# Kernel optimization log

Hardware: AMD Instinct MI355X
Metric: run time of the kernel (lower is better)

## Reference

```python
import jax, jax.numpy as jnp
import numpy as np

T, B, I, H, C, O = 4096, 8, 256, 512, 1024, 512
SCHEDULE = 1.0
UPPER_T = 0.3
NIND = int((1.0 - SCHEDULE) * (C - 2) * UPPER_T) + 1  # = 1 (argmax WTA)


def setup_inputs() -> dict:
    key = jax.random.key(0)
    ks = jax.random.split(key, 8)
    def lin(k, fan_out, fan_in):
        s = 1.0 / np.sqrt(fan_in)
        kw, kb = jax.random.split(k)
        return (jax.random.uniform(kw, (fan_out, fan_in), jnp.float32, -s, s),
                jax.random.uniform(kb, (fan_out,), jnp.float32, -s, s))
    i2m_w, i2m_b = lin(ks[0], H, I)
    m2h_w, m2h_b = lin(ks[1], C, H)
    h2o_w, h2o_b = lin(ks[2], O, C)
    return {
        "x": jax.random.normal(ks[3], (T, B, I), jnp.float32),
        "hidden1": jnp.zeros((1,), jnp.float32),  # unused dummy (overwritten in torch forward)
        "i2m_w": i2m_w, "i2m_b": i2m_b,
        "m2h_w": m2h_w, "m2h_b": m2h_b,
        "h2o_w": h2o_w, "h2o_b": h2o_b,
    }


def reference(x, hidden1, i2m_w, i2m_b, m2h_w, m2h_b, h2o_w, h2o_b):
    # linear -> relu
    h = jax.nn.relu(jnp.einsum('tbi,hi->tbh', x, i2m_w) + i2m_b)
    # linear -> relu -> concept pre-activations [T,B,C]
    c = jax.nn.relu(jnp.einsum('tbh,ch->tbc', h, m2h_w) + m2h_b)
    # winner-take-all: top-Nind scatter mask (replaces CPU argsort round-trip)
    _, idx = jax.lax.top_k(c, NIND)  # [T,B,NIND]
    t_ix = jnp.arange(c.shape[0])[:, None, None]
    b_ix = jnp.arange(c.shape[1])[None, :, None]
    mask = jnp.zeros_like(c).at[t_ix, b_ix, idx].set(1.0)
    m = c * mask
    # L2 normalize over concept axis
    m = m / jnp.linalg.norm(m, axis=-1, keepdims=True)
    out = jnp.einsum('tbc,oc->tbo', m, h2o_w) + h2o_b
    return jax.nn.log_softmax(out, axis=-1)
```

## Files before the change

kernel.cpp:

```cpp
#include <hip/hip_runtime.h>
#include <stdint.h>

#define M_ROWS 32768
#define I_DIM 256
#define H_DIM 512
#define C_DIM 1024
#define O_DIM 512

typedef __attribute__((ext_vector_type(8))) short bf16x8;
typedef __attribute__((ext_vector_type(4))) float f32x4;

__device__ __forceinline__ ushort bf16_rne(float f) {
    unsigned u = __float_as_uint(f);
    unsigned r = u + 0x7FFFu + ((u >> 16) & 1u);
    return (ushort)(r >> 16);
}
__device__ __forceinline__ float bf16_f32(ushort h) {
    return __uint_as_float(((unsigned)h) << 16);
}
__device__ __forceinline__ void split2(float f, ushort& hi, ushort& mid) {
    hi = bf16_rne(f);
    mid = bf16_rne(f - bf16_f32(hi));
}

__device__ __forceinline__ void async_ld16(const void* g, void* l) {
    __builtin_amdgcn_global_load_lds(
        (const __attribute__((address_space(1))) void*)g,
        (__attribute__((address_space(3))) void*)l, 16, 0, 0);
}

__device__ __forceinline__ unsigned long long packvi(float v, int col) {
    unsigned u = __float_as_uint(v);
    u = (u & 0x80000000u) ? ~u : (u | 0x80000000u);
    return ((unsigned long long)u << 32) | (unsigned)(~col);
}

__device__ __forceinline__ int slot_of(int kc, int row) {
    return (kc + ((row >> 1) & 3)) & 3;
}

__global__ __launch_bounds__(256)
void prep(const float* __restrict__ W1, ushort* __restrict__ w1h, ushort* __restrict__ w1m,
          const float* __restrict__ W2, ushort* __restrict__ w2h, ushort* __restrict__ w2m,
          const float* __restrict__ Wo, const float* __restrict__ bo,
          float* __restrict__ LS, unsigned long long* __restrict__ part) {
    __shared__ float sred[4];
    const int b = blockIdx.x;
    const int t = threadIdx.x;
    if (b < 320) {
        const int isW1 = (b < 64);
        const float* W = isW1 ? W1 : W2;
        ushort* hh = isW1 ? w1h : w2h;
        ushort* mm = isW1 ? w1m : w2m;
        const int K = isW1 ? I_DIM : H_DIM;
        const int cpr = K >> 3;
        int gid = (isW1 ? b : b - 64) * 256 + t;
        int row = gid / cpr;
        int rem = gid - row * cpr;
        int g = rem >> 2, kc = rem & 3;
        float4 v0 = *(const float4*)(W + (size_t)gid * 8);
        float4 v1 = *(const float4*)(W + (size_t)gid * 8 + 4);
        __align__(16) ushort h[8], m[8];
        float f[8];
        *(float4*)&f[0] = v0; *(float4*)&f[4] = v1;
        #pragma unroll
        for (int j = 0; j < 8; ++j) split2(f[j], h[j], m[j]);
        size_t dst = (size_t)row * K + g * 32 + slot_of(kc, row) * 8;
        *(uint4*)(hh + dst) = *(uint4*)h;
        *(uint4*)(mm + dst) = *(uint4*)m;
    } else if (b < 1344) {
        const int j = b - 320;
        float l0 = Wo[(size_t)t * C_DIM + j] + bo[t];
        float l1 = Wo[(size_t)(t + 256) * C_DIM + j] + bo[t + 256];

        float mx = fmaxf(l0, l1);
        #pragma unroll
        for (int off = 1; off < 64; off <<= 1)
            mx = fmaxf(mx, __shfl_xor(mx, off, 64));
        if ((t & 63) == 0) sred[t >> 6] = mx;
        __syncthreads();
        mx = fmaxf(fmaxf(sred[0], sred[1]), fmaxf(sred[2], sred[3]));
        __syncthreads();

        float s = expf(l0 - mx) + expf(l1 - mx);
        #pragma unroll
        for (int off = 1; off < 64; off <<= 1)
            s += __shfl_xor(s, off, 64);
        if ((t & 63) == 0) sred[t >> 6] = s;
        __syncthreads();
        s = sred[0] + sred[1] + sred[2] + sred[3];

        float lse = mx + logf(s);
        LS[(size_t)j * O_DIM + t] = l0 - lse;
        LS[(size_t)j * O_DIM + t + 256] = l1 - lse;
    } else {
        part[(b - 1344) * 256 + t] = 0ull;
    }
}

__global__ __launch_bounds__(256, 4)
void gemm1_mfma(const float* __restrict__ X, const ushort* __restrict__ W1h,
                const ushort* __restrict__ W1m, const float* __restrict__ b1,
                ushort* __restrict__ Hh, ushort* __restrict__ Hm) {
    __shared__ __align__(16) ushort LB[16384];
    ushort* As0 = LB;
    ushort* As1 = LB + 4096;
    ushort* Bs0 = LB + 8192;
    ushort* Bs1 = LB + 12288;

    const int tid = threadIdx.x;
    const int lane = tid & 63, wave = tid >> 6;
    const int wm = wave >> 1, wn = wave & 1;
    const int lcol = lane & 15, quad = lane >> 4;
    const int mBase = blockIdx.x * 128;
    const int nBase = blockIdx.y * 128;
    const int s_row = tid >> 1, s_half = tid & 1;
    const int bplane = wave >> 1;
    const ushort* wp = bplane ? W1m : W1h;
    const int brow0 = (wave & 1) * 64;
    const int lrow = lane >> 2, lk = (lane & 3) * 8;

    f32x4 acc[4][4];
    #pragma unroll
    for (int i = 0; i < 4; ++i)
        #pragma unroll
        for (int j = 0; j < 4; ++j)
            acc[i][j] = (f32x4){0.f, 0.f, 0.f, 0.f};

    int aoff[4], boff[4];
    #pragma unroll
    for (int t = 0; t < 4; ++t) {
        int ra = wm * 64 + t * 16 + lcol;
        int rb = wn * 64 + t * 16 + lcol;
        aoff[t] = ra * 32 + slot_of(quad, ra) * 8;
        boff[t] = rb * 32 + slot_of(quad, rb) * 8;
    }
    const int sl0 = slot_of(s_half * 2,     s_row);
    const int sl1 = slot_of(s_half * 2 + 1, s_row);

    for (int ks = 0; ks < I_DIM / 32; ++ks) {
        const int k0 = ks * 32;
        const float* ap = X + (size_t)(mBase + s_row) * I_DIM + k0 + s_half * 16;
        float4 f0 = ((const float4*)ap)[0];
        float4 f1 = ((const float4*)ap)[1];
        float4 f2 = ((const float4*)ap)[2];
        float4 f3 = ((const float4*)ap)[3];

        __syncthreads();

        #pragma unroll
        for (int i = 0; i < 4; ++i) {
            int r = brow0 + i * 16;
            const ushort* g = wp + (size_t)(nBase + r + lrow) * I_DIM + k0 + lk;
            async_ld16(g, (bplane ? Bs1 : Bs0) + r * 32);
        }

        float f[16];
        *(float4*)&f[0] = f0; *(float4*)&f[4] = f1;
        *(float4*)&f[8] = f2; *(float4*)&f[12] = f3;
        bf16x8 h0, h1, m0, m1;
        #pragma unroll
        for (int j = 0; j < 8; ++j) {
            ushort hu, mu;
            split2(f[j], hu, mu);
            h0[j] = (short)hu; m0[j] = (short)mu;
            split2(f[j + 8], hu, mu);
            h1[j] = (short)hu; m1[j] = (short)mu;
        }
        *(bf16x8*)&As0[s_row * 32 + sl0 * 8] = h0;
        *(bf16x8*)&As0[s_row * 32 + sl1 * 8] = h1;
        *(bf16x8*)&As1[s_row * 32 + sl0 * 8] = m0;
        *(bf16x8*)&As1[s_row * 32 + sl1 * 8] = m1;

        __syncthreads();

        bf16x8 af[4][2];
        #pragma unroll
        for (int mt = 0; mt < 4; ++mt) {
            af[mt][0] = *(const bf16x8*)&As0[aoff[mt]];
            af[mt][1] = *(const bf16x8*)&As1[aoff[mt]];
        }
        #pragma unroll
        for (int nt = 0; nt < 4; ++nt) {
            bf16x8 bh = *(const bf16x8*)&Bs0[boff[nt]];
            bf16x8 bm = *(const bf16x8*)&Bs1[boff[nt]];
            #pragma unroll
            for (int mt = 0; mt < 4; ++mt) {
                f32x4 a = acc[mt][nt];
                a = __builtin_amdgcn_mfma_f32_16x16x32_bf16(af[mt][1], bh, a, 0, 0, 0);
                a = __builtin_amdgcn_mfma_f32_16x16x32_bf16(af[mt][0], bm, a, 0, 0, 0);
                a = __builtin_amdgcn_mfma_f32_16x16x32_bf16(af[mt][0], bh, a, 0, 0, 0);
                acc[mt][nt] = a;
            }
        }
    }

    #pragma unroll
    for (int plane = 0; plane < 2; ++plane) {
        __syncthreads();
        #pragma unroll
        for (int nt = 0; nt < 4; ++nt) {
            int colRel = wn * 64 + nt * 16 + lcol;
            int g = colRel >> 5, kc = (colRel >> 3) & 3, pos = colRel & 7;
            float bias = b1[nBase + colRel];
            #pragma unroll
            for (int mt = 0; mt < 4; ++mt) {
                #pragma unroll
                for (int r = 0; r < 4; ++r) {
                    int rowRel = wm * 64 + mt * 16 + quad * 4 + r;
                    float v = fmaxf(acc[mt][nt][r] + bias, 0.f);
                    ushort hu, mu;
                    split2(v, hu, mu);
                    LB[rowRel * 128 + g * 32 + slot_of(kc, rowRel) * 8 + pos]
                        = plane ? mu : hu;
                }
            }
        }
        __syncthreads();
        ushort* dstp = plane ? Hm : Hh;
        #pragma unroll
        for (int l = 0; l < 8; ++l) {
            int c = l * 256 + tid;
            int row = c >> 4, idx = c & 15;
            *(uint4*)(dstp + (size_t)(mBase + row) * H_DIM + nBase + idx * 8)
                = *(const uint4*)&LB[row * 128 + idx * 8];
        }
    }
}

__global__ __launch_bounds__(256, 4)
void gemm2_mfma(const ushort* __restrict__ Hh, const ushort* __restrict__ Hm,
                const ushort* __restrict__ W2h, const ushort* __restrict__ W2m,
                const float* __restrict__ b2,
                unsigned long long* __restrict__ part) {
    __shared__ __align__(16) ushort As[2][128 * 32];
    __shared__ __align__(16) ushort Bs[2][128 * 32];
    const int tid = threadIdx.x;
    const int lane = tid & 63, wave = tid >> 6;
    const int wm = wave >> 1, wn = wave & 1;
    const int lcol = lane & 15, quad = lane >> 4;
    const int mBase = blockIdx.x * 128;
    const int nBase = blockIdx.y * 128;
    const int lrow = lane >> 2, lk = (lane & 3) * 8;

    const ushort* gsrc;
    ushort* lbase;
    switch (wave) {
        case 0: gsrc = Hh  + (size_t)mBase * H_DIM; lbase = As[0]; break;
        case 1: gsrc = Hm  + (size_t)mBase * H_DIM; lbase = As[1]; break;
        case 2: gsrc = W2h + (size_t)nBase * H_DIM; lbase = Bs[0]; break;
        default: gsrc = W2m + (size_t)nBase * H_DIM; lbase = Bs[1]; break;
    }

    f32x4 acc[4][4];
    #pragma unroll
    for (int i = 0; i < 4; ++i)
        #pragma unroll
        for (int j = 0; j < 4; ++j)
            acc[i][j] = (f32x4){0.f, 0.f, 0.f, 0.f};

    int aoff[4], boff[4];
    #pragma unroll
    for (int t = 0; t < 4; ++t) {
        int ra = wm * 64 + t * 16 + lcol;
        int rb = wn * 64 + t * 16 + lcol;
        aoff[t] = ra * 32 + slot_of(quad, ra) * 8;
        boff[t] = rb * 32 + slot_of(quad, rb) * 8;
    }

    for (int ks = 0; ks < H_DIM / 32; ++ks) {
        const int k0 = ks * 32;
        __syncthreads();
        #pragma unroll
        for (int j = 0; j < 8; ++j) {
            const ushort* g = gsrc + (size_t)(j * 16 + lrow) * H_DIM + k0 + lk;
            async_ld16(g, lbase + j * 512);
        }
        __syncthreads();

        bf16x8 af[4][2];
        #pragma unroll
        for (int mt = 0; mt < 4; ++mt) {
            af[mt][0] = *(const bf16x8*)&As[0][aoff[mt]];
            af[mt][1] = *(const bf16x8*)&As[1][aoff[mt]];
        }
        #pragma unroll
        for (int nt = 0; nt < 4; ++nt) {
            bf16x8 bh = *(const bf16x8*)&Bs[0][boff[nt]];
            bf16x8 bm = *(const bf16x8*)&Bs[1][boff[nt]];
            #pragma unroll
            for (int mt = 0; mt < 4; ++mt) {
                f32x4 a = acc[mt][nt];
                a = __builtin_amdgcn_mfma_f32_16x16x32_bf16(af[mt][1], bh, a, 0, 0, 0);
                a = __builtin_amdgcn_mfma_f32_16x16x32_bf16(af[mt][0], bm, a, 0, 0, 0);
                a = __builtin_amdgcn_mfma_f32_16x16x32_bf16(af[mt][0], bh, a, 0, 0, 0);
                acc[mt][nt] = a;
            }
        }
    }

    #pragma unroll
    for (int mt = 0; mt < 4; ++mt) {
        #pragma unroll
        for (int r = 0; r < 4; ++r) {
            unsigned long long best = 0ull;
            #pragma unroll
            for (int nt = 0; nt < 4; ++nt) {
                int col = nBase + wn * 64 + nt * 16 + lcol;
                float v = acc[mt][nt][r] + b2[col];
                unsigned long long p = packvi(v, col);
                if (p > best) best = p;
            }
            #pragma unroll
            for (int off = 1; off < 16; off <<= 1) {
                unsigned long long o = __shfl_xor((long long)best, off, 64);
                if (o > best) best = o;
            }
            if (lcol == 0) {
                int row = mBase + wm * 64 + mt * 16 + quad * 4 + r;
                atomicMax(&part[row], best);
            }
        }
    }
}

__global__ __launch_bounds__(256)
void gather_out(const unsigned long long* __restrict__ part,
                const float* __restrict__ LS, float* __restrict__ out) {
    const int tid = threadIdx.x;
    const int row = blockIdx.x * 2 + (tid >> 7);
    const int q = tid & 127;
    unsigned long long best = part[row];
    unsigned u = (unsigned)(best >> 32);
    float v = (u & 0x80000000u) ? __uint_as_float(u ^ 0x80000000u)
                                : __uint_as_float(~u);
    int col = (int)(~(unsigned)best) & (C_DIM - 1);
    int j = (v > 0.f) ? col : 0;
    float4 val = ((const float4*)LS)[(size_t)j * 128 + q];
    ((float4*)out)[(size_t)row * 128 + q] = val;
}

extern "C" void kernel_launch(void* const* d_in, const int* in_sizes, int n_in,
                              void* d_out, int out_size, void* d_ws, size_t ws_size,
                              hipStream_t stream) {
    const float* x     = (const float*)d_in[0];
    const float* i2m_w = (const float*)d_in[2];
    const float* i2m_b = (const float*)d_in[3];
    const float* m2h_w = (const float*)d_in[4];
    const float* m2h_b = (const float*)d_in[5];
    const float* h2o_w = (const float*)d_in[6];
    const float* h2o_b = (const float*)d_in[7];
    float* out = (float*)d_out;

    char* ws = (char*)d_ws;
    ushort* w1h = (ushort*)(ws);
    ushort* w1m = (ushort*)(ws + 262144);
    ushort* w2h = (ushort*)(ws + 524288);
    ushort* w2m = (ushort*)(ws + 1572864);
    float*  LS  = (float*)(ws + 2621440);
    unsigned long long* part = (unsigned long long*)(ws + 4718592);

    ushort* Hh = (ushort*)d_out;
    ushort* Hm = Hh + (size_t)M_ROWS * H_DIM;

    prep<<<1472, 256, 0, stream>>>(i2m_w, w1h, w1m, m2h_w, w2h, w2m,
                                   h2o_w, h2o_b, LS, part);
    gemm1_mfma<<<dim3(M_ROWS / 128, H_DIM / 128), 256, 0, stream>>>(
        x, w1h, w1m, i2m_b, Hh, Hm);
    gemm2_mfma<<<dim3(M_ROWS / 128, C_DIM / 128), 256, 0, stream>>>(
        Hh, Hm, w2h, w2m, m2h_b, part);
    gather_out<<<M_ROWS / 2, 256, 0, stream>>>(part, LS, out);
}
```

Measured before the change: 253.5 us.

## Double-buffer LDS in both GEMMs, swap grid order, restructure logsoftmax prep

Both MFMA GEMMs now use double-buffered shared memory. The next K-slice is loaded asynchronously, and in gemm1 the next X slice is prefetched into registers, while MFMAs run on the current buffer. This removes one barrier per iteration and overlaps loads with compute. The grid is transposed so that consecutive blocks share the same M rows across N tiles, which should improve L2 reuse of the activation rows. Launch bounds drop to 2 waves/SIMD because LDS use doubles. The output log-softmax table in prep now handles 16 columns per block with coalesced reads, cutting the prep grid from 1472 to 512 blocks.

```diff
diff --git a/kernel.cpp b/kernel.cpp
--- a/kernel.cpp
+++ b/kernel.cpp
@@ -44,7 +44,7 @@
           const float* __restrict__ W2, ushort* __restrict__ w2h, ushort* __restrict__ w2m,
           const float* __restrict__ Wo, const float* __restrict__ bo,
           float* __restrict__ LS, unsigned long long* __restrict__ part) {
-    __shared__ float sred[4];
+    __shared__ float red[16][17];
     const int b = blockIdx.x;
     const int t = threadIdx.x;
     if (b < 320) {
@@ -68,52 +68,58 @@
         size_t dst = (size_t)row * K + g * 32 + slot_of(kc, row) * 8;
         *(uint4*)(hh + dst) = *(uint4*)h;
         *(uint4*)(mm + dst) = *(uint4*)m;
-    } else if (b < 1344) {
-        const int j = b - 320;
-        float l0 = Wo[(size_t)t * C_DIM + j] + bo[t];
-        float l1 = Wo[(size_t)(t + 256) * C_DIM + j] + bo[t + 256];
-
-        float mx = fmaxf(l0, l1);
-        #pragma unroll
-        for (int off = 1; off < 64; off <<= 1)
-            mx = fmaxf(mx, __shfl_xor(mx, off, 64));
-        if ((t & 63) == 0) sred[t >> 6] = mx;
-        __syncthreads();
-        mx = fmaxf(fmaxf(sred[0], sred[1]), fmaxf(sred[2], sred[3]));
-        __syncthreads();
-
-        float s = expf(l0 - mx) + expf(l1 - mx);
-        #pragma unroll
-        for (int off = 1; off < 64; off <<= 1)
-            s += __shfl_xor(s, off, 64);
-        if ((t & 63) == 0) sred[t >> 6] = s;
-        __syncthreads();
-        s = sred[0] + sred[1] + sred[2] + sred[3];
-
-        float lse = mx + logf(s);
-        LS[(size_t)j * O_DIM + t] = l0 - lse;
-        LS[(size_t)j * O_DIM + t + 256] = l1 - lse;
+    } else if (b < 384) {
+        const int j0 = (b - 320) * 16;
+        const int c = t & 15, q = t >> 4;
+        float v[32];
+        float mx = -3.4e38f;
+        #pragma unroll
+        for (int i = 0; i < 32; ++i) {
+            int r = q + 16 * i;
+            v[i] = Wo[(size_t)r * C_DIM + j0 + c] + bo[r];
+            mx = fmaxf(mx, v[i]);
+        }
+        red[q][c] = mx;
+        __syncthreads();
+        #pragma unroll
+        for (int s = 8; s > 0; s >>= 1) {
+            if (q < s) red[q][c] = fmaxf(red[q][c], red[q + s][c]);
+            __syncthreads();
+        }
+        mx = red[0][c];
+        __syncthreads();
+        float sum = 0.f;
+        #pragma unroll
+        for (int i = 0; i < 32; ++i) sum += expf(v[i] - mx);
+        red[q][c] = sum;
+        __syncthreads();
+        #pragma unroll
+        for (int s = 8; s > 0; s >>= 1) {
+            if (q < s) red[q][c] += red[q + s][c];
+            __syncthreads();
+        }
+        float lse = mx + logf(red[0][c]);
+        #pragma unroll
+        for (int i = 0; i < 32; ++i)
+            LS[(size_t)(j0 + c) * O_DIM + q + 16 * i] = v[i] - lse;
     } else {
-        part[(b - 1344) * 256 + t] = 0ull;
-    }
-}
-
-__global__ __launch_bounds__(256, 4)
+        part[(b - 384) * 256 + t] = 0ull;
+    }
+}
+
+__global__ __launch_bounds__(256, 2)
 void gemm1_mfma(const float* __restrict__ X, const ushort* __restrict__ W1h,
                 const ushort* __restrict__ W1m, const float* __restrict__ b1,
                 ushort* __restrict__ Hh, ushort* __restrict__ Hm) {
-    __shared__ __align__(16) ushort LB[16384];
-    ushort* As0 = LB;
-    ushort* As1 = LB + 4096;
-    ushort* Bs0 = LB + 8192;
-    ushort* Bs1 = LB + 12288;
+    __shared__ __align__(16) ushort As[2][2][4096];
+    __shared__ __align__(16) ushort Bs[2][2][4096];
 
     const int tid = threadIdx.x;
     const int lane = tid & 63, wave = tid >> 6;
     const int wm = wave >> 1, wn = wave & 1;
     const int lcol = lane & 15, quad = lane >> 4;
-    const int mBase = blockIdx.x * 128;
-    const int nBase = blockIdx.y * 128;
+    const int nBase = blockIdx.x * 128;
+    const int mBase = blockIdx.y * 128;
     const int s_row = tid >> 1, s_half = tid & 1;
     const int bplane = wave >> 1;
     const ushort* wp = bplane ? W1m : W1h;
@@ -137,27 +143,15 @@
     }
     const int sl0 = slot_of(s_half * 2,     s_row);
     const int sl1 = slot_of(s_half * 2 + 1, s_row);
-
-    for (int ks = 0; ks < I_DIM / 32; ++ks) {
-        const int k0 = ks * 32;
-        const float* ap = X + (size_t)(mBase + s_row) * I_DIM + k0 + s_half * 16;
-        float4 f0 = ((const float4*)ap)[0];
-        float4 f1 = ((const float4*)ap)[1];
-        float4 f2 = ((const float4*)ap)[2];
-        float4 f3 = ((const float4*)ap)[3];
-
-        __syncthreads();
-
-        #pragma unroll
-        for (int i = 0; i < 4; ++i) {
-            int r = brow0 + i * 16;
-            const ushort* g = wp + (size_t)(nBase + r + lrow) * I_DIM + k0 + lk;
-            async_ld16(g, (bplane ? Bs1 : Bs0) + r * 32);
-        }
-
+    const float* xrow = X + (size_t)(mBase + s_row) * I_DIM + s_half * 16;
+
+    float4 xr[2][4];
+    #pragma unroll
+    for (int i = 0; i < 4; ++i) xr[0][i] = ((const float4*)xrow)[i];
+    {
         float f[16];
-        *(float4*)&f[0] = f0; *(float4*)&f[4] = f1;
-        *(float4*)&f[8] = f2; *(float4*)&f[12] = f3;
+        #pragma unroll
+        for (int i = 0; i < 4; ++i) *(float4*)&f[i * 4] = xr[0][i];
         bf16x8 h0, h1, m0, m1;
         #pragma unroll
         for (int j = 0; j < 8; ++j) {
@@ -167,23 +161,64 @@
             split2(f[j + 8], hu, mu);
             h1[j] = (short)hu; m1[j] = (short)mu;
         }
-        *(bf16x8*)&As0[s_row * 32 + sl0 * 8] = h0;
-        *(bf16x8*)&As0[s_row * 32 + sl1 * 8] = h1;
-        *(bf16x8*)&As1[s_row * 32 + sl0 * 8] = m0;
-        *(bf16x8*)&As1[s_row * 32 + sl1 * 8] = m1;
-
-        __syncthreads();
+        *(bf16x8*)&As[0][0][s_row * 32 + sl0 * 8] = h0;
+        *(bf16x8*)&As[0][0][s_row * 32 + sl1 * 8] = h1;
+        *(bf16x8*)&As[0][1][s_row * 32 + sl0 * 8] = m0;
+        *(bf16x8*)&As[0][1][s_row * 32 + sl1 * 8] = m1;
+    }
+    #pragma unroll
+    for (int i = 0; i < 4; ++i) {
+        int r = brow0 + i * 16;
+        async_ld16(wp + (size_t)(nBase + r + lrow) * I_DIM + lk, &Bs[0][bplane][r * 32]);
+    }
+    #pragma unroll
+    for (int i = 0; i < 4; ++i) xr[1][i] = ((const float4*)(xrow + 32))[i];
+
+    #pragma unroll 2
+    for (int ks = 0; ks < 8; ++ks) {
+        const int cur = ks & 1;
+        __syncthreads();
+        if (ks < 7) {
+            const int k0 = (ks + 1) * 32;
+            #pragma unroll
+            for (int i = 0; i < 4; ++i) {
+                int r = brow0 + i * 16;
+                async_ld16(wp + (size_t)(nBase + r + lrow) * I_DIM + k0 + lk,
+                           &Bs[cur ^ 1][bplane][r * 32]);
+            }
+            float f[16];
+            #pragma unroll
+            for (int i = 0; i < 4; ++i) *(float4*)&f[i * 4] = xr[(ks + 1) & 1][i];
+            bf16x8 h0, h1, m0, m1;
+            #pragma unroll
+            for (int j = 0; j < 8; ++j) {
+                ushort hu, mu;
+                split2(f[j], hu, mu);
+                h0[j] = (short)hu; m0[j] = (short)mu;
+                split2(f[j + 8], hu, mu);
+                h1[j] = (short)hu; m1[j] = (short)mu;
+            }
+            *(bf16x8*)&As[cur ^ 1][0][s_row * 32 + sl0 * 8] = h0;
+            *(bf16x8*)&As[cur ^ 1][0][s_row * 32 + sl1 * 8] = h1;
+            *(bf16x8*)&As[cur ^ 1][1][s_row * 32 + sl0 * 8] = m0;
+            *(bf16x8*)&As[cur ^ 1][1][s_row * 32 + sl1 * 8] = m1;
+        }
+        if (ks < 6) {
+            const float* xp = xrow + (ks + 2) * 32;
+            #pragma unroll
+            for (int i = 0; i < 4; ++i) xr[ks & 1][i] = ((const float4*)xp)[i];
+        }
 
         bf16x8 af[4][2];
         #pragma unroll
         for (int mt = 0; mt < 4; ++mt) {
-            af[mt][0] = *(const bf16x8*)&As0[aoff[mt]];
-            af[mt][1] = *(const bf16x8*)&As1[aoff[mt]];
+            af[mt][0] = *(const bf16x8*)&As[cur][0][aoff[mt]];
+            af[mt][1] = *(const bf16x8*)&As[cur][1][aoff[mt]];
         }
         #pragma unroll
         for (int nt = 0; nt < 4; ++nt) {
-            bf16x8 bh = *(const bf16x8*)&Bs0[boff[nt]];
-            bf16x8 bm = *(const bf16x8*)&Bs1[boff[nt]];
+            bf16x8 bh = *(const bf16x8*)&Bs[cur][0][boff[nt]];
+            bf16x8 bm = *(const bf16x8*)&Bs[cur][1][boff[nt]];
             #pragma unroll
             for (int mt = 0; mt < 4; ++mt) {
                 f32x4 a = acc[mt][nt];
@@ -195,6 +230,7 @@
         }
     }
 
+    ushort* LB = &As[0][0][0];
     #pragma unroll
     for (int plane = 0; plane < 2; ++plane) {
         __syncthreads();
@@ -228,28 +264,28 @@
     }
 }
 
-__global__ __launch_bounds__(256, 4)
+__global__ __launch_bounds__(256, 2)
 void gemm2_mfma(const ushort* __restrict__ Hh, const ushort* __restrict__ Hm,
                 const ushort* __restrict__ W2h, const ushort* __restrict__ W2m,
                 const float* __restrict__ b2,
                 unsigned long long* __restrict__ part) {
-    __shared__ __align__(16) ushort As[2][128 * 32];
-    __shared__ __align__(16) ushort Bs[2][128 * 32];
+    __shared__ __align__(16) ushort As[2][2][4096];
+    __shared__ __align__(16) ushort Bs[2][2][4096];
     const int tid = threadIdx.x;
     const int lane = tid & 63, wave = tid >> 6;
     const int wm = wave >> 1, wn = wave & 1;
     const int lcol = lane & 15, quad = lane >> 4;
-    const int mBase = blockIdx.x * 128;
-    const int nBase = blockIdx.y * 128;
+    const int nBase = blockIdx.x * 128;
+    const int mBase = blockIdx.y * 128;
     const int lrow = lane >> 2, lk = (lane & 3) * 8;
 
     const ushort* gsrc;
-    ushort* lbase;
+    ushort *lb0, *lb1;
     switch (wave) {
-        case 0: gsrc = Hh  + (size_t)mBase * H_DIM; lbase = As[0]; break;
-        case 1: gsrc = Hm  + (size_t)mBase * H_DIM; lbase = As[1]; break;
-        case 2: gsrc = W2h + (size_t)nBase * H_DIM; lbase = Bs[0]; break;
-        default: gsrc = W2m + (size_t)nBase * H_DIM; lbase = Bs[1]; break;
+        case 0: gsrc = Hh  + (size_t)mBase * H_DIM; lb0 = As[0][0]; lb1 = As[1][0]; break;
+        case 1: gsrc = Hm  + (size_t)mBase * H_DIM; lb0 = As[0][1]; lb1 = As[1][1]; break;
+        case 2: gsrc = W2h + (size_t)nBase * H_DIM; lb0 = Bs[0][0]; lb1 = Bs[1][0]; break;
+        default: gsrc = W2m + (size_t)nBase * H_DIM; lb0 = Bs[0][1]; lb1 = Bs[1][1]; break;
     }
 
     f32x4 acc[4][4];
@@ -268,26 +304,33 @@
         boff[t] = rb * 32 + slot_of(quad, rb) * 8;
     }
 
-    for (int ks = 0; ks < H_DIM / 32; ++ks) {
-        const int k0 = ks * 32;
-        __syncthreads();
-        #pragma unroll
-        for (int j = 0; j < 8; ++j) {
-            const ushort* g = gsrc + (size_t)(j * 16 + lrow) * H_DIM + k0 + lk;
-            async_ld16(g, lbase + j * 512);
-        }
-        __syncthreads();
+    #pragma unroll
+    for (int j = 0; j < 8; ++j)
+        async_ld16(gsrc + (size_t)(j * 16 + lrow) * H_DIM + lk, lb0 + j * 512);
+
+    #pragma unroll 2
+    for (int ks = 0; ks < 16; ++ks) {
+        const int cur = ks & 1;
+        __syncthreads();
+        if (ks < 15) {
+            const int k0 = (ks + 1) * 32;
+            ushort* lb = cur ? lb0 : lb1;
+            #pragma unroll
+            for (int j = 0; j < 8; ++j)
+                async_ld16(gsrc + (size_t)(j * 16 + lrow) * H_DIM + k0 + lk,
+                           lb + j * 512);
+        }
 
         bf16x8 af[4][2];
         #pragma unroll
         for (int mt = 0; mt < 4; ++mt) {
-            af[mt][0] = *(const bf16x8*)&As[0][aoff[mt]];
-            af[mt][1] = *(const bf16x8*)&As[1][aoff[mt]];
+            af[mt][0] = *(const bf16x8*)&As[cur][0][aoff[mt]];
+            af[mt][1] = *(const bf16x8*)&As[cur][1][aoff[mt]];
         }
         #pragma unroll
         for (int nt = 0; nt < 4; ++nt) {
-            bf16x8 bh = *(const bf16x8*)&Bs[0][boff[nt]];
-            bf16x8 bm = *(const bf16x8*)&Bs[1][boff[nt]];
+            bf16x8 bh = *(const bf16x8*)&Bs[cur][0][boff[nt]];
+            bf16x8 bm = *(const bf16x8*)&Bs[cur][1][boff[nt]];
             #pragma unroll
             for (int mt = 0; mt < 4; ++mt) {
                 f32x4 a = acc[mt][nt];
@@ -363,11 +406,11 @@
     ushort* Hh = (ushort*)d_out;
     ushort* Hm = Hh + (size_t)M_ROWS * H_DIM;
 
-    prep<<<1472, 256, 0, stream>>>(i2m_w, w1h, w1m, m2h_w, w2h, w2m,
-                                   h2o_w, h2o_b, LS, part);
-    gemm1_mfma<<<dim3(M_ROWS / 128, H_DIM / 128), 256, 0, stream>>>(
+    prep<<<512, 256, 0, stream>>>(i2m_w, w1h, w1m, m2h_w, w2h, w2m,
+                                  h2o_w, h2o_b, LS, part);
+    gemm1_mfma<<<dim3(H_DIM / 128, M_ROWS / 128), 256, 0, stream>>>(
         x, w1h, w1m, i2m_b, Hh, Hm);
-    gemm2_mfma<<<dim3(M_ROWS / 128, C_DIM / 128), 256, 0, stream>>>(
+    gemm2_mfma<<<dim3(C_DIM / 128, M_ROWS / 128), 256, 0, stream>>>(
         Hh, Hm, w2h, w2m, m2h_b, part);
     gather_out<<<M_ROWS / 2, 256, 0, stream>>>(part, LS, out);
 }
```

New measurement: 273.4 us. 1.08x slower.

## Double-buffer gemm2 with 128x64 tiles and batch logit-softmax prep per block

Applied to the files above, without the earlier changes.

gemm2 now loads the next K slice into a second LDS buffer while the current one feeds MFMAs, so each step needs one barrier instead of two. The N tile shrinks from 128 to 64, which doubles the grid and halves accumulator registers, and launch bounds drop to 3 blocks per CU. The prep softmax for precomputed output logits now handles 16 concept columns per block, giving coalesced column reads and 64 blocks instead of 1024. The trade-offs are that A tiles are reloaded twice as often across N, and each block uses more LDS.

```diff
diff --git a/kernel.cpp b/kernel.cpp
--- a/kernel.cpp
+++ b/kernel.cpp
@@ -44,7 +44,7 @@
           const float* __restrict__ W2, ushort* __restrict__ w2h, ushort* __restrict__ w2m,
           const float* __restrict__ Wo, const float* __restrict__ bo,
           float* __restrict__ LS, unsigned long long* __restrict__ part) {
-    __shared__ float sred[4];
+    __shared__ float red[16][17];
     const int b = blockIdx.x;
     const int t = threadIdx.x;
     if (b < 320) {
@@ -68,33 +68,42 @@
         size_t dst = (size_t)row * K + g * 32 + slot_of(kc, row) * 8;
         *(uint4*)(hh + dst) = *(uint4*)h;
         *(uint4*)(mm + dst) = *(uint4*)m;
-    } else if (b < 1344) {
-        const int j = b - 320;
-        float l0 = Wo[(size_t)t * C_DIM + j] + bo[t];
-        float l1 = Wo[(size_t)(t + 256) * C_DIM + j] + bo[t + 256];
-
-        float mx = fmaxf(l0, l1);
-        #pragma unroll
-        for (int off = 1; off < 64; off <<= 1)
-            mx = fmaxf(mx, __shfl_xor(mx, off, 64));
-        if ((t & 63) == 0) sred[t >> 6] = mx;
-        __syncthreads();
-        mx = fmaxf(fmaxf(sred[0], sred[1]), fmaxf(sred[2], sred[3]));
-        __syncthreads();
-
-        float s = expf(l0 - mx) + expf(l1 - mx);
-        #pragma unroll
-        for (int off = 1; off < 64; off <<= 1)
-            s += __shfl_xor(s, off, 64);
-        if ((t & 63) == 0) sred[t >> 6] = s;
-        __syncthreads();
-        s = sred[0] + sred[1] + sred[2] + sred[3];
-
-        float lse = mx + logf(s);
-        LS[(size_t)j * O_DIM + t] = l0 - lse;
-        LS[(size_t)j * O_DIM + t + 256] = l1 - lse;
+    } else if (b < 384) {
+        const int j0 = (b - 320) * 16;
+        const int c = t & 15, q = t >> 4;
+        float v[32];
+        float mx = -3.4e38f;
+        #pragma unroll
+        for (int i = 0; i < 32; ++i) {
+            int r = q + 16 * i;
+            v[i] = Wo[(size_t)r * C_DIM + j0 + c] + bo[r];
+            mx = fmaxf(mx, v[i]);
+        }
+        red[q][c] = mx;
+        __syncthreads();
+        #pragma unroll
+        for (int s = 8; s > 0; s >>= 1) {
+            if (q < s) red[q][c] = fmaxf(red[q][c], red[q + s][c]);
+            __syncthreads();
+        }
+        mx = red[0][c];
+        __syncthreads();
+        float sum = 0.f;
+        #pragma unroll
+        for (int i = 0; i < 32; ++i) sum += expf(v[i] - mx);
+        red[q][c] = sum;
+        __syncthreads();
+        #pragma unroll
+        for (int s = 8; s > 0; s >>= 1) {
+            if (q < s) red[q][c] += red[q + s][c];
+            __syncthreads();
+        }
+        float lse = mx + logf(red[0][c]);
+        #pragma unroll
+        for (int i = 0; i < 32; ++i)
+            LS[(size_t)(j0 + c) * O_DIM + q + 16 * i] = v[i] - lse;
     } else {
-        part[(b - 1344) * 256 + t] = 0ull;
+        part[(b - 384) * 256 + t] = 0ull;
     }
 }
 
@@ -228,66 +237,88 @@
     }
 }
 
-__global__ __launch_bounds__(256, 4)
+__global__ __launch_bounds__(256, 3)
 void gemm2_mfma(const ushort* __restrict__ Hh, const ushort* __restrict__ Hm,
                 const ushort* __restrict__ W2h, const ushort* __restrict__ W2m,
                 const float* __restrict__ b2,
                 unsigned long long* __restrict__ part) {
-    __shared__ __align__(16) ushort As[2][128 * 32];
-    __shared__ __align__(16) ushort Bs[2][128 * 32];
+    __shared__ __align__(16) ushort As[2][2][128 * 32];
+    __shared__ __align__(16) ushort Bs[2][2][64 * 32];
     const int tid = threadIdx.x;
     const int lane = tid & 63, wave = tid >> 6;
     const int wm = wave >> 1, wn = wave & 1;
     const int lcol = lane & 15, quad = lane >> 4;
     const int mBase = blockIdx.x * 128;
-    const int nBase = blockIdx.y * 128;
+    const int nBase = blockIdx.y * 64;
     const int lrow = lane >> 2, lk = (lane & 3) * 8;
 
     const ushort* gsrc;
-    ushort* lbase;
+    ushort *lb0, *lb1;
     switch (wave) {
-        case 0: gsrc = Hh  + (size_t)mBase * H_DIM; lbase = As[0]; break;
-        case 1: gsrc = Hm  + (size_t)mBase * H_DIM; lbase = As[1]; break;
-        case 2: gsrc = W2h + (size_t)nBase * H_DIM; lbase = Bs[0]; break;
-        default: gsrc = W2m + (size_t)nBase * H_DIM; lbase = Bs[1]; break;
-    }
-
-    f32x4 acc[4][4];
+        case 0:  gsrc = Hh  + (size_t)mBase * H_DIM; lb0 = As[0][0]; lb1 = As[1][0]; break;
+        case 1:  gsrc = Hm  + (size_t)mBase * H_DIM; lb0 = As[0][1]; lb1 = As[1][1]; break;
+        case 2:  gsrc = W2h + (size_t)nBase * H_DIM; lb0 = Bs[0][0]; lb1 = Bs[1][0]; break;
+        default: gsrc = W2m + (size_t)nBase * H_DIM; lb0 = Bs[0][1]; lb1 = Bs[1][1]; break;
+    }
+    const int isA = (wave < 2);
+
+    f32x4 acc[4][2];
     #pragma unroll
     for (int i = 0; i < 4; ++i)
         #pragma unroll
-        for (int j = 0; j < 4; ++j)
+        for (int j = 0; j < 2; ++j)
             acc[i][j] = (f32x4){0.f, 0.f, 0.f, 0.f};
 
-    int aoff[4], boff[4];
+    int aoff[4], boff[2];
     #pragma unroll
     for (int t = 0; t < 4; ++t) {
         int ra = wm * 64 + t * 16 + lcol;
-        int rb = wn * 64 + t * 16 + lcol;
         aoff[t] = ra * 32 + slot_of(quad, ra) * 8;
+    }
+    #pragma unroll
+    for (int t = 0; t < 2; ++t) {
+        int rb = wn * 32 + t * 16 + lcol;
         boff[t] = rb * 32 + slot_of(quad, rb) * 8;
     }
 
-    for (int ks = 0; ks < H_DIM / 32; ++ks) {
-        const int k0 = ks * 32;
-        __syncthreads();
-        #pragma unroll
-        for (int j = 0; j < 8; ++j) {
-            const ushort* g = gsrc + (size_t)(j * 16 + lrow) * H_DIM + k0 + lk;
-            async_ld16(g, lbase + j * 512);
-        }
-        __syncthreads();
+    #pragma unroll
+    for (int j = 0; j < 4; ++j)
+        async_ld16(gsrc + (size_t)(j * 16 + lrow) * H_DIM + lk, lb0 + j * 512);
+    if (isA) {
+        #pragma unroll
+        for (int j = 4; j < 8; ++j)
+            async_ld16(gsrc + (size_t)(j * 16 + lrow) * H_DIM + lk, lb0 + j * 512);
+    }
+
+    #pragma unroll 2
+    for (int ks = 0; ks < 16; ++ks) {
+        const int cur = ks & 1;
+        __syncthreads();
+        if (ks < 15) {
+            const int k0 = (ks + 1) * 32;
+            ushort* lb = cur ? lb0 : lb1;
+            #pragma unroll
+            for (int j = 0; j < 4; ++j)
+                async_ld16(gsrc + (size_t)(j * 16 + lrow) * H_DIM + k0 + lk,
+                           lb + j * 512);
+            if (isA) {
+                #pragma unroll
+                for (int j = 4; j < 8; ++j)
+                    async_ld16(gsrc + (size_t)(j * 16 + lrow) * H_DIM + k0 + lk,
+                               lb + j * 512);
+            }
+        }
 
         bf16x8 af[4][2];
         #pragma unroll
         for (int mt = 0; mt < 4; ++mt) {
-            af[mt][0] = *(const bf16x8*)&As[0][aoff[mt]];
-            af[mt][1] = *(const bf16x8*)&As[1][aoff[mt]];
-        }
-        #pragma unroll
-        for (int nt = 0; nt < 4; ++nt) {
-            bf16x8 bh = *(const bf16x8*)&Bs[0][boff[nt]];
-            bf16x8 bm = *(const bf16x8*)&Bs[1][boff[nt]];
+            af[mt][0] = *(const bf16x8*)&As[cur][0][aoff[mt]];
+            af[mt][1] = *(const bf16x8*)&As[cur][1][aoff[mt]];
+        }
+        #pragma unroll
+        for (int nt = 0; nt < 2; ++nt) {
+            bf16x8 bh = *(const bf16x8*)&Bs[cur][0][boff[nt]];
+            bf16x8 bm = *(const bf16x8*)&Bs[cur][1][boff[nt]];
             #pragma unroll
             for (int mt = 0; mt < 4; ++mt) {
                 f32x4 a = acc[mt][nt];
@@ -305,8 +336,8 @@
         for (int r = 0; r < 4; ++r) {
             unsigned long long best = 0ull;
             #pragma unroll
-            for (int nt = 0; nt < 4; ++nt) {
-                int col = nBase + wn * 64 + nt * 16 + lcol;
+            for (int nt = 0; nt < 2; ++nt) {
+                int col = nBase + wn * 32 + nt * 16 + lcol;
                 float v = acc[mt][nt][r] + b2[col];
                 unsigned long long p = packvi(v, col);
                 if (p > best) best = p;
@@ -363,11 +394,11 @@
     ushort* Hh = (ushort*)d_out;
     ushort* Hm = Hh + (size_t)M_ROWS * H_DIM;
 
-    prep<<<1472, 256, 0, stream>>>(i2m_w, w1h, w1m, m2h_w, w2h, w2m,
-                                   h2o_w, h2o_b, LS, part);
+    prep<<<512, 256, 0, stream>>>(i2m_w, w1h, w1m, m2h_w, w2h, w2m,
+                                  h2o_w, h2o_b, LS, part);
     gemm1_mfma<<<dim3(M_ROWS / 128, H_DIM / 128), 256, 0, stream>>>(
         x, w1h, w1m, i2m_b, Hh, Hm);
-    gemm2_mfma<<<dim3(M_ROWS / 128, C_DIM / 128), 256, 0, stream>>>(
+    gemm2_mfma<<<dim3(M_ROWS / 128, C_DIM / 64), 256, 0, stream>>>(
         Hh, Hm, w2h, w2m, m2h_b, part);
     gather_out<<<M_ROWS / 2, 256, 0, stream>>>(part, LS, out);
 }
```

Result: slower. 309.8 us (+22.2%).
